# Kernel optimization log

Measured on AMD Instinct MI355X. Metric: run time of the kernel, lower is better.

The kernel has to match this reference:

```python
import jax, jax.numpy as jnp
import numpy as np

P = 2  # lrtd_pad (p_l == p_r == p_t == p_d)
B, C, H, W = 4, 64, 128, 128


def setup_inputs() -> dict:
    key = jax.random.key(0)
    x = jax.random.normal(key, (B, 6, C, H, W), dtype=jnp.float32)
    return {"x": x}


def _cube_pad(x):
    # faces: [B,C,H,W] each; order matches torch module unpacking
    fb, fd, ff, fl, fr, ft = (x[:, i] for i in range(6))
    flip_h = lambda a: a[:, :, ::-1, :]   # flip along dim 2 (rows)
    flip_w = lambda a: a[:, :, :, ::-1]   # flip along dim 3 (cols)
    T = lambda a: jnp.swapaxes(a, 2, 3)   # permute(0,1,3,2)

    # top strips for faces 0..5 -> [B,6,C,P,W]
    top = jnp.stack([
        flip_h(ft[:, :, :P, :]),           # back
        ff[:, :, -P:, :],                  # down
        ft[:, :, -P:, :],                  # front
        T(ft[:, :, :, :P]),                # left
        flip_h(T(ft[:, :, :, -P:])),       # right
        flip_h(fb[:, :, :P, :]),           # top
    ], axis=1)

    # bottom strips -> [B,6,C,P,W]
    bot = jnp.stack([
        flip_h(fd[:, :, -P:, :]),
        flip_h(fb[:, :, -P:, :]),
        fd[:, :, :P, :],
        flip_h(T(fd[:, :, :, :P])),
        T(fd[:, :, :, -P:]),
        ff[:, :, :P, :],
    ], axis=1)

    # left strips -> [B,6,C,H,P]
    lft = jnp.stack([
        fr[:, :, :, -P:],
        flip_w(T(fl[:, :, -P:, :])),
        fl[:, :, :, -P:],
        fb[:, :, :, -P:],
        ff[:, :, :, -P:],
        T(fl[:, :, :P, :]),
    ], axis=1)

    # right strips -> [B,6,C,H,P]
    rgt = jnp.stack([
        fl[:, :, :, :P],
        T(fr[:, :, -P:, :]),
        fr[:, :, :, :P],
        ff[:, :, :, :P],
        fb[:, :, :, :P],
        flip_w(T(fr[:, :, :P, :])),
    ], axis=1)

    # corners: equal pads -> repeat the top/bottom strip's edge column along width
    p_tl = jnp.tile(top[:, :, :, :P, :1], (1, 1, 1, 1, P))
    p_tr = jnp.tile(top[:, :, :, -P:, -1:], (1, 1, 1, 1, P))
    p_dl = jnp.tile(bot[:, :, :, :P, :1], (1, 1, 1, 1, P))
    p_dr = jnp.tile(bot[:, :, :, -P:, -1:], (1, 1, 1, 1, P))

    mid = jnp.concatenate([top, x, bot], axis=3)            # [B,6,C,H+2P,W]
    left = jnp.concatenate([p_tl, lft, p_dl], axis=3)       # [B,6,C,H+2P,P]
    right = jnp.concatenate([p_tr, rgt, p_dr], axis=3)      # [B,6,C,H+2P,P]
    return jnp.concatenate([left, mid, right], axis=4)      # [B,6,C,H+2P,W+2P]


def reference(x):
    return _cube_pad(x)
```

## Files before the change

kernel.cpp:

```cpp
#include <hip/hip_runtime.h>


constexpr int P = 2, B = 4, C = 64, H = 128, W = 128;
constexpr int Ho = H + 2 * P, Wo = W + 2 * P;
constexpr int NV = Wo / 4;
constexpr int PLANES = B * 6 * C;
constexpr int PER_PLANE = Ho * NV;

typedef float vfloat4 __attribute__((ext_vector_type(4)));
typedef vfloat4 float4u __attribute__((aligned(4)));

__device__ __forceinline__ void top_map(int f, int t, int w, int& sf, int& r, int& col) {
    switch (f) {
        case 0:  sf = 5; r = P - 1 - t; col = w;         break;
        case 1:  sf = 2; r = H - P + t; col = w;         break;
        case 2:  sf = 5; r = H - P + t; col = w;         break;
        case 3:  sf = 5; r = w;         col = t;         break;
        case 4:  sf = 5; r = w;         col = W - 1 - t; break;
        default: sf = 0; r = P - 1 - t; col = w;         break;
    }
}
__device__ __forceinline__ void bot_map(int f, int t, int w, int& sf, int& r, int& col) {
    switch (f) {
        case 0:  sf = 1; r = H - 1 - t; col = w;         break;
        case 1:  sf = 0; r = H - 1 - t; col = w;         break;
        case 2:  sf = 1; r = t;         col = w;         break;
        case 3:  sf = 1; r = w;         col = P - 1 - t; break;
        case 4:  sf = 1; r = w;         col = W - P + t; break;
        default: sf = 2; r = t;         col = w;         break;
    }
}
__device__ __forceinline__ void lft_map(int f, int h, int l, int& sf, int& r, int& col) {
    switch (f) {
        case 0:  sf = 4; r = h;         col = W - P + l; break;
        case 1:  sf = 3; r = H - 1 - l; col = h;         break;
        case 2:  sf = 3; r = h;         col = W - P + l; break;
        case 3:  sf = 0; r = h;         col = W - P + l; break;
        case 4:  sf = 2; r = h;         col = W - P + l; break;
        default: sf = 3; r = l;         col = h;         break;
    }
}
__device__ __forceinline__ void rgt_map(int f, int h, int rr, int& sf, int& r, int& col) {
    switch (f) {
        case 0:  sf = 3; r = h;          col = rr;        break;
        case 1:  sf = 4; r = H - P + rr; col = h;         break;
        case 2:  sf = 4; r = h;          col = rr;        break;
        case 3:  sf = 2; r = h;          col = rr;        break;
        case 4:  sf = 0; r = h;          col = rr;        break;
        default: sf = 4; r = P - 1 - rr; col = h;         break;
    }
}
__device__ __forceinline__ void gen_map(int f, int i, int j, int& sf, int& r, int& col) {
    bool in_h = (i >= P) && (i < H + P);
    bool in_w = (j >= P) && (j < W + P);
    if (in_h && in_w) {
        sf = f; r = i - P; col = j - P;
    } else if (!in_h) {
        int w = in_w ? (j - P) : (j < P ? 0 : W - 1);
        if (i < P) top_map(f, i, w, sf, r, col);
        else       bot_map(f, i - H - P, w, sf, r, col);
    } else {
        if (j < P) lft_map(f, i - P, j,         sf, r, col);
        else       rgt_map(f, i - P, j - W - P, sf, r, col);
    }
}

__global__ __launch_bounds__(256) void cubepad_p_kernel(const float* __restrict__ x,
                                                        float* __restrict__ out) {
    const int plane = blockIdx.y;
    const int f  = (plane / C) % 6;
    const int bC = plane - f * C;
    const float* __restrict__ xp = x + (size_t)plane * (H * W);
    float*       __restrict__ op = out + (size_t)plane * (Ho * Wo);

    int tx = blockIdx.x * 256 + threadIdx.x;
    if (tx >= PER_PLANE) return;
    int i = tx / NV;
    int v = tx - i * NV;

    float4 val;
    bool fast = (i >= P) && (i < H + P) && (v >= 1) && (v < NV - 1);
    if (fast) {
        const float* s = xp + (i - P) * W + (4 * v - P);
        float4u t = *(const float4u*)s;
        val = make_float4(t.x, t.y, t.z, t.w);
    } else {
        float* vp = (float*)&val;
        #pragma unroll
        for (int e = 0; e < 4; ++e) {
            int sf, r, col;
            gen_map(f, i, 4 * v + e, sf, r, col);
            vp[e] = x[((size_t)(bC + sf * C)) * (H * W) + (size_t)r * W + col];
        }
    }
    *(float4*)(op + i * Wo + 4 * v) = val;
}

extern "C" void kernel_launch(void* const* d_in, const int* in_sizes, int n_in,
                              void* d_out, int out_size, void* d_ws, size_t ws_size,
                              hipStream_t stream) {
    const float* x = (const float*)d_in[0];
    float* out = (float*)d_out;
    dim3 grid((PER_PLANE + 255) / 256, PLANES);
    cubepad_p_kernel<<<grid, 256, 0, stream>>>(x, out);
}
```

Measured before the change: 186.3 us.

## Process all four batches per thread with flattened 1D grid

Each thread now handles the same slot across all four batch elements, issuing four independent vector loads and stores per thread, and the 2D grid becomes a flat 1D grid over planes within one batch. The goal is more memory-level parallelism per thread, amortised index and face-mapping arithmetic, and no partial tail blocks per plane. The cost is a quarter as many threads, which lowers occupancy for a purely bandwidth-bound copy, and it relies on SLOTS dividing evenly by 256.

```diff
diff --git a/kernel.cpp b/kernel.cpp
--- a/kernel.cpp
+++ b/kernel.cpp
@@ -4,8 +4,11 @@
 constexpr int P = 2, B = 4, C = 64, H = 128, W = 128;
 constexpr int Ho = H + 2 * P, Wo = W + 2 * P;
 constexpr int NV = Wo / 4;
-constexpr int PLANES = B * 6 * C;
-constexpr int PER_PLANE = Ho * NV;
+constexpr int PPB = 6 * C;
+constexpr int SLOTS_PER_PLANE = Ho * NV;
+constexpr int SLOTS = PPB * SLOTS_PER_PLANE;
+constexpr size_t BSI = (size_t)PPB * H * W;
+constexpr size_t BSO = (size_t)PPB * Ho * Wo;
 
 typedef float vfloat4 __attribute__((ext_vector_type(4)));
 typedef vfloat4 float4u __attribute__((aligned(4)));
@@ -65,35 +68,47 @@
     }
 }
 
-__global__ __launch_bounds__(256) void cubepad_p_kernel(const float* __restrict__ x,
-                                                        float* __restrict__ out) {
-    const int plane = blockIdx.y;
-    const int f  = (plane / C) % 6;
-    const int bC = plane - f * C;
-    const float* __restrict__ xp = x + (size_t)plane * (H * W);
-    float*       __restrict__ op = out + (size_t)plane * (Ho * Wo);
+__global__ __launch_bounds__(256) void cubepad_b4_kernel(const float* __restrict__ x,
+                                                         float* __restrict__ out) {
+    int slot = blockIdx.x * 256 + threadIdx.x;
+    int pib  = slot / SLOTS_PER_PLANE;
+    int rem  = slot - pib * SLOTS_PER_PLANE;
+    int i    = rem / NV;
+    int v    = rem - i * NV;
 
-    int tx = blockIdx.x * 256 + threadIdx.x;
-    if (tx >= PER_PLANE) return;
-    int i = tx / NV;
-    int v = tx - i * NV;
+    const float* __restrict__ xp = x   + (size_t)pib * (H * W);
+    float*       __restrict__ op = out + (size_t)pib * (Ho * Wo);
 
-    float4 val;
     bool fast = (i >= P) && (i < H + P) && (v >= 1) && (v < NV - 1);
     if (fast) {
         const float* s = xp + (i - P) * W + (4 * v - P);
-        float4u t = *(const float4u*)s;
-        val = make_float4(t.x, t.y, t.z, t.w);
+        float4u t0 = *(const float4u*)(s);
+        float4u t1 = *(const float4u*)(s + BSI);
+        float4u t2 = *(const float4u*)(s + 2 * BSI);
+        float4u t3 = *(const float4u*)(s + 3 * BSI);
+        float* o = op + i * Wo + 4 * v;
+        *(vfloat4*)(o)           = t0;
+        *(vfloat4*)(o + BSO)     = t1;
+        *(vfloat4*)(o + 2 * BSO) = t2;
+        *(vfloat4*)(o + 3 * BSO) = t3;
     } else {
-        float* vp = (float*)&val;
+        int f = pib / C;
+        int c = pib - f * C;
+        float4 val[4];
         #pragma unroll
         for (int e = 0; e < 4; ++e) {
             int sf, r, col;
             gen_map(f, i, 4 * v + e, sf, r, col);
-            vp[e] = x[((size_t)(bC + sf * C)) * (H * W) + (size_t)r * W + col];
+            size_t so = ((size_t)(sf * C + c)) * (H * W) + (size_t)r * W + col;
+            #pragma unroll
+            for (int b = 0; b < 4; ++b)
+                ((float*)&val[b])[e] = x[so + b * BSI];
         }
+        float* o = op + i * Wo + 4 * v;
+        #pragma unroll
+        for (int b = 0; b < 4; ++b)
+            *(float4*)(o + b * BSO) = val[b];
     }
-    *(float4*)(op + i * Wo + 4 * v) = val;
 }
 
 extern "C" void kernel_launch(void* const* d_in, const int* in_sizes, int n_in,
@@ -101,6 +116,5 @@
                               hipStream_t stream) {
     const float* x = (const float*)d_in[0];
     float* out = (float*)d_out;
-    dim3 grid((PER_PLANE + 255) / 256, PLANES);
-    cubepad_p_kernel<<<grid, 256, 0, stream>>>(x, out);
+    cubepad_b4_kernel<<<SLOTS / 256, 256, 0, stream>>>(x, out);
 }
```

Result: slower. 200.9 us (+7.8%).
